# Kernel tuning notes

Measured on AMD Instinct MI355X. Metric: run time of the kernel, lower is better.

## Reference

```python
import jax, jax.numpy as jnp
import numpy as np

N, E, F, H, L = 10000, 200000, 28, 256, 6
NUM_ATOM, NUM_BOND = 100, 24

def ssp(x):
    # shifted softplus used by SchNet
    return jax.nn.softplus(x) - jnp.log(2.0)

def setup_inputs() -> dict:
    key = jax.random.key(0)
    ks = iter(jax.random.split(key, 64))
    def nrm(shape, scale=0.05):
        return jax.random.normal(next(ks), shape, dtype=jnp.float32) * scale
    inp = {}
    inp['atom_type'] = jax.random.randint(next(ks), (N,), 0, NUM_ATOM)
    inp['r_feat'] = jax.random.normal(next(ks), (N, F), dtype=jnp.float32)
    inp['p_feat'] = jax.random.normal(next(ks), (N, F), dtype=jnp.float32)
    inp['pos'] = jax.random.normal(next(ks), (N, 3), dtype=jnp.float32) * 3.0
    inp['edge_index'] = jax.random.randint(next(ks), (2, E), 0, N)
    inp['edge_type_r'] = jax.random.randint(next(ks), (E,), 0, NUM_BOND)
    inp['edge_type_p'] = jax.random.randint(next(ks), (E,), 0, NUM_BOND)
    # learned parameters
    inp['atom_emb_table'] = nrm((NUM_ATOM, H // 2), 1.0)
    inp['feat_W'] = nrm((F, H // 2))                       # atom_feat_embedding (no bias)
    inp['bond_emb_table'] = nrm((NUM_BOND, H), 1.0)        # edge encoder bond embedding
    inp['edge_mlp_W1'] = nrm((1, H)); inp['edge_mlp_b1'] = jnp.zeros((H,), jnp.float32)
    inp['edge_mlp_W2'] = nrm((H, H)); inp['edge_mlp_b2'] = jnp.zeros((H,), jnp.float32)
    inp['cat_W1'] = nrm((2 * H, H)); inp['cat_b1'] = jnp.zeros((H,), jnp.float32)
    inp['cat_W2'] = nrm((H, H)); inp['cat_b2'] = jnp.zeros((H,), jnp.float32)
    # SchNet interaction blocks, stacked over L layers
    inp['filt_W1'] = nrm((L, H, H)); inp['filt_b1'] = jnp.zeros((L, H), jnp.float32)
    inp['filt_W2'] = nrm((L, H, H)); inp['filt_b2'] = jnp.zeros((L, H), jnp.float32)
    inp['lin1_W'] = nrm((L, H, H))
    inp['lin2_W'] = nrm((L, H, H)); inp['lin2_b'] = jnp.zeros((L, H), jnp.float32)
    inp['lin3_W'] = nrm((L, H, H)); inp['lin3_b'] = jnp.zeros((L, H), jnp.float32)
    # grad_global_dist_mlp: 2H -> H -> H/2 -> 1
    inp['grad_W1'] = nrm((2 * H, H)); inp['grad_b1'] = jnp.zeros((H,), jnp.float32)
    inp['grad_W2'] = nrm((H, H // 2)); inp['grad_b2'] = jnp.zeros((H // 2,), jnp.float32)
    inp['grad_W3'] = nrm((H // 2, 1)); inp['grad_b3'] = jnp.zeros((1,), jnp.float32)
    return inp

def _forward(r_feat, p_feat, pos, atom_emb_table, feat_W, bond_emb_table,
             edge_mlp_W1, edge_mlp_b1, edge_mlp_W2, edge_mlp_b2,
             cat_W1, cat_b1, cat_W2, cat_b2,
             filt_W1, filt_b1, filt_W2, filt_b2,
             lin1_W, lin2_W, lin2_b, lin3_W, lin3_b,
             grad_W1, grad_b1, grad_W2, grad_b2, grad_W3, grad_b3,
             atom_type, edge_index, edge_type_r, edge_type_p):
    src, dst = edge_index[0], edge_index[1]
    # node embedding: z = [atom_emb + feat(r), feat(p) - feat(r)]
    ar = r_feat @ feat_W
    ap = p_feat @ feat_W
    z = jnp.concatenate([atom_emb_table[atom_type] + ar, ap - ar], axis=-1)  # (N, H)
    # edge lengths (E, 1)
    d = pos[src] - pos[dst]
    edge_length = jnp.sqrt(jnp.sum(d * d, axis=-1, keepdims=True) + 1e-12)
    # condensed edge embedding 'bond_w_d': mlp(d) * bond_emb(type), r/p branches, then edge_cat MLP
    d_emb = ssp(edge_length @ edge_mlp_W1 + edge_mlp_b1) @ edge_mlp_W2 + edge_mlp_b2  # (E, H)
    attr_r = d_emb * bond_emb_table[edge_type_r]
    attr_p = d_emb * bond_emb_table[edge_type_p]
    edge_attr = jax.nn.relu(jnp.concatenate([attr_r, attr_p], -1) @ cat_W1 + cat_b1) @ cat_W2 + cat_b2  # (E, H)
    # SchNet encoder: L CFConv interaction blocks with residual
    nn_ = z.shape[0]
    def layer(h, p):
        fW1, fb1, fW2, fb2, l1, l2, l2b, l3, l3b = p
        Wf = ssp(edge_attr @ fW1 + fb1) @ fW2 + fb2            # (E, H) continuous filters
        msg = (h @ l1)[src] * Wf                               # gather + modulate
        agg = jax.ops.segment_sum(msg, dst, num_segments=nn_)  # scatter-add to nodes
        return h + (ssp(agg @ l2 + l2b) @ l3 + l3b), None
    node_attr, _ = jax.lax.scan(layer, z, (filt_W1, filt_b1, filt_W2, filt_b2, lin1_W, lin2_W, lin2_b, lin3_W, lin3_b))
    # assemble_atom_pair_feature: [h_row * h_col, edge_attr] -> (E, 2H)
    h_pair = jnp.concatenate([node_attr[src] * node_attr[dst], edge_attr], axis=-1)
    h = jax.nn.relu(h_pair @ grad_W1 + grad_b1)
    h = jax.nn.relu(h @ grad_W2 + grad_b2)
    edge_inv = h @ grad_W3 + grad_b3                           # (E, 1)
    return edge_inv, edge_length

def reference(atom_type, r_feat, p_feat, pos, edge_index, edge_type_r, edge_type_p,
              atom_emb_table, feat_W, bond_emb_table,
              edge_mlp_W1, edge_mlp_b1, edge_mlp_W2, edge_mlp_b2,
              cat_W1, cat_b1, cat_W2, cat_b2,
              filt_W1, filt_b1, filt_W2, filt_b2,
              lin1_W, lin2_W, lin2_b, lin3_W, lin3_b,
              grad_W1, grad_b1, grad_W2, grad_b2, grad_W3, grad_b3):
    return _forward(r_feat, p_feat, pos, atom_emb_table, feat_W, bond_emb_table,
                    edge_mlp_W1, edge_mlp_b1, edge_mlp_W2, edge_mlp_b2,
                    cat_W1, cat_b1, cat_W2, cat_b2,
                    filt_W1, filt_b1, filt_W2, filt_b2,
                    lin1_W, lin2_W, lin2_b, lin3_W, lin3_b,
                    grad_W1, grad_b1, grad_W2, grad_b2, grad_W3, grad_b3,
                    atom_type, edge_index, edge_type_r, edge_type_p)
```

## Files before the change

kernel.cpp:

```cpp
#include <hip/hip_runtime.h>
#include <hip/hip_bf16.h>
#include <math.h>

#define HDIM 256

typedef unsigned short u16;
typedef short short8 __attribute__((ext_vector_type(8)));
typedef _Float16 f16x8 __attribute__((ext_vector_type(8)));
typedef float f32x4 __attribute__((ext_vector_type(4)));

__device__ __forceinline__ float sspf(float x) {
  const float LOG2E = 1.4426950408889634f, LN2 = 0.6931471805599453f;
  float t = exp2f(-fabsf(x) * LOG2E);
  return fmaxf(x, 0.f) + (log2f(1.f + t) - 1.f) * LN2;
}
__device__ __forceinline__ float bf2f(u16 u) {
  union { unsigned int i; float f; } x; x.i = ((unsigned int)u) << 16; return x.f;
}
__device__ __forceinline__ u16 f2bf(float f) {
  union { float f; unsigned int i; } x; x.f = f;
  unsigned int r = x.i + 0x7FFFu + ((x.i >> 16) & 1u);
  return (u16)(r >> 16);
}
__device__ __forceinline__ u16 f2h_bits(float f) {
  _Float16 h = (_Float16)f;
  return __builtin_bit_cast(unsigned short, h);
}
__device__ __forceinline__ float4 ld4f(const float* p) { return *(const float4*)p; }

__device__ __forceinline__ int iw_idx(int row, int col) {
  return row * 256 + ((((col >> 3) ^ (row & 7)) << 3) | (col & 7));
}
__device__ __forceinline__ int ir_idx(int row, int cchunk) {
  return row * 256 + ((cchunk ^ (row & 7)) << 3);
}

template<int DT>
__device__ __forceinline__ f32x4 mma(short8 a, short8 b, f32x4 c) {
  if constexpr (DT == 0)
    return __builtin_amdgcn_mfma_f32_16x16x32_bf16(a, b, c, 0, 0, 0);
  else
    return __builtin_amdgcn_mfma_f32_16x16x32_f16(__builtin_bit_cast(f16x8, a),
                                                  __builtin_bit_cast(f16x8, b), c, 0, 0, 0);
}

__device__ __forceinline__ void zacc(f32x4 (&acc)[4][4]) {
#pragma unroll
  for (int i = 0; i < 4; ++i)
#pragma unroll
    for (int j = 0; j < 4; ++j) { acc[i][j][0]=0.f; acc[i][j][1]=0.f; acc[i][j][2]=0.f; acc[i][j][3]=0.f; }
}

template<int NSTEPS, int BT_N, int NTW, int DT, bool WRAP8, typename ATR>
__device__ __forceinline__ void gemm44(f32x4 (&acc)[4][4], const u16* __restrict__ bt,
                                       const u16* __restrict__ inter,
                                       int w, int m, int quad, ATR atr) {
  short8 bf[2][NTW];
#pragma unroll
  for (int nt = 0; nt < NTW; ++nt)
    bf[0][nt] = *(const short8*)(bt + (w * (NTW * 16) + nt * 16 + m) * 32 + quad * 8);
#pragma unroll
  for (int ks = 0; ks < NSTEPS; ++ks) {
    const int cur = ks & 1, nxt = cur ^ 1;
    if (ks + 1 < NSTEPS) {
#pragma unroll
      for (int nt = 0; nt < NTW; ++nt)
        bf[nxt][nt] = *(const short8*)(bt + (size_t)(ks + 1) * (BT_N * 32)
                                       + (w * (NTW * 16) + nt * 16 + m) * 32 + quad * 8);
    }
    int kchunk = (WRAP8 ? (ks & 7) : ks) * 4 + quad;
#pragma unroll
    for (int mt = 0; mt < 4; ++mt) {
      short8 af = *(const short8*)&inter[ir_idx(mt * 16 + m, kchunk)];
      af = atr(mt, ks, af);
#pragma unroll
      for (int nt = 0; nt < NTW; ++nt)
        acc[mt][nt] = mma<DT>(af, bf[cur][nt], acc[mt][nt]);
    }
  }
}

template<int NTW, int ACT, int OF>
__device__ __forceinline__ void store_inter44(u16* inter, int w, int m, int quad,
                                              const f32x4 (&acc)[4][4], const float* bias) {
#pragma unroll
  for (int mt = 0; mt < 4; ++mt)
#pragma unroll
    for (int nt = 0; nt < NTW; ++nt) {
      int col = w * (NTW * 16) + nt * 16 + m;
      float bv = bias[col];
#pragma unroll
      for (int r = 0; r < 4; ++r) {
        int row = mt * 16 + quad * 4 + r;
        float x = acc[mt][nt][r] + bv;
        if (ACT == 1) x = fmaxf(x, 0.f);
        else if (ACT == 2) x = sspf(x);
        inter[iw_idx(row, col)] = (OF == 0) ? f2bf(x) : f2h_bits(x);
      }
    }
}

__device__ __forceinline__ void copy_out(u16* C, int row0, const u16* inter, int t) {
#pragma unroll
  for (int c = 0; c < 8; ++c) {
    int idx = c * 256 + t;
    int row = idx >> 5, c8 = idx & 31;
    int src = (c8 ^ (row & 7)) << 3;
    *(short8*)(C + (size_t)(row0 + row) * HDIM + c8 * 8) = *(const short8*)&inter[row * 256 + src];
  }
}

template<int NTW, int ACT, int CM>
__device__ __forceinline__ void store_node44(float* C, int row0, int w, int m, int quad,
                                             const f32x4 (&acc)[4][4], const float* bias, int M) {
#pragma unroll
  for (int mt = 0; mt < 4; ++mt)
#pragma unroll
    for (int nt = 0; nt < NTW; ++nt) {
      int col = w * (NTW * 16) + nt * 16 + m;
      float bv = bias ? bias[col] : 0.f;
#pragma unroll
      for (int r = 0; r < 4; ++r) {
        int row = row0 + mt * 16 + quad * 4 + r;
        if (row < M) {
          float x = acc[mt][nt][r] + bv;
          if (ACT == 2) x = sspf(x);
          size_t idx = (size_t)row * HDIM + col;
          if (CM == 1) x += C[idx];
          C[idx] = x;
        }
      }
    }
}

struct EncArgs {
  const int* se_e; const float* lenp; const float* W1; const float* b1;
  const u16* btA; const float* bA;
  const float* bondT; const int* etr; const int* etp;
  const u16* btB; const float* bB;
  const u16* btC; const float* bC;
  u16* outp;
};
__global__ __launch_bounds__(256, 3) void encoder_k(EncArgs a) {
  __shared__ u16 inter[64 * 256];
  __shared__ u16 bondL[24 * 264];
  const int t = threadIdx.x;
  const int w = t >> 6, lane = t & 63, m = lane & 15, quad = lane >> 4;
  const int row0 = blockIdx.x * 64;
  auto idt = [](int, int, short8 v) { return v; };

  for (int i = t; i < 24 * 256; i += 256) {
    int r = i >> 8, c = i & 255;
    bondL[r * 264 + c] = f2h_bits(a.bondT[r * 256 + c]);
  }
  int brv[4], bpv[4];
#pragma unroll
  for (int mt = 0; mt < 4; ++mt) {
    int eo = a.se_e[row0 + mt * 16 + m];
    brv[mt] = a.etr[eo]; bpv[mt] = a.etp[eo];
  }
  {
    int row = t >> 2;
    float len = a.lenp[a.se_e[row0 + row]];
#pragma unroll
    for (int c = 0; c < 8; ++c) {
      int chunk = (t & 3) + c * 4, k = chunk * 8;
      float4 w0 = ld4f(a.W1 + k), w1 = ld4f(a.W1 + k + 4);
      float4 c0 = ld4f(a.b1 + k), c1 = ld4f(a.b1 + k + 4);
      short8 v;
      v[0] = (short)f2bf(sspf(len * w0.x + c0.x)); v[1] = (short)f2bf(sspf(len * w0.y + c0.y));
      v[2] = (short)f2bf(sspf(len * w0.z + c0.z)); v[3] = (short)f2bf(sspf(len * w0.w + c0.w));
      v[4] = (short)f2bf(sspf(len * w1.x + c1.x)); v[5] = (short)f2bf(sspf(len * w1.y + c1.y));
      v[6] = (short)f2bf(sspf(len * w1.z + c1.z)); v[7] = (short)f2bf(sspf(len * w1.w + c1.w));
      *(short8*)&inter[row * 256 + ((chunk ^ (row & 7)) << 3)] = v;
    }
  }
  __syncthreads();
  f32x4 acc[4][4];
  zacc(acc);
  gemm44<8, 256, 4, 0, false>(acc, a.btA, inter, w, m, quad, idt);
  __syncthreads();
  store_inter44<4, 0, 1>(inter, w, m, quad, acc, a.bA);
  __syncthreads();
  zacc(acc);
  auto atrB = [&](int mt, int ks, short8 v) -> short8 {
    int k2 = (ks & 7) * 32 + quad * 8;
    int et = (ks < 8) ? brv[mt] : bpv[mt];
    f16x8 dv = __builtin_bit_cast(f16x8, v);
    f16x8 bd = __builtin_bit_cast(f16x8, *(const short8*)&bondL[et * 264 + k2]);
    return __builtin_bit_cast(short8, dv * bd);
  };
  gemm44<16, 256, 4, 1, true>(acc, a.btB, inter, w, m, quad, atrB);
  __syncthreads();
  store_inter44<4, 1, 0>(inter, w, m, quad, acc, a.bB);
  __syncthreads();
  zacc(acc);
  gemm44<8, 256, 4, 0, false>(acc, a.btC, inter, w, m, quad, idt);
  __syncthreads();
  store_inter44<4, 0, 0>(inter, w, m, quad, acc, a.bC);
  __syncthreads();
  copy_out(a.outp, row0, inter, t);
}

struct FL1Args {
  const u16* eA; const u16* bt1; const float* b1; const u16* bt2; const float* b2; u16* Wf;
  int EBlocks;
  const float* h; const u16* btL; float* hh; int M;
};
__global__ __launch_bounds__(256, 3) void fl1_k(FL1Args a) {
  __shared__ u16 inter[64 * 256];
  const int t = threadIdx.x;
  const int w = t >> 6, lane = t & 63, m = lane & 15, quad = lane >> 4;
  auto idt = [](int, int, short8 v) { return v; };
  if ((int)blockIdx.x < a.EBlocks) {
    const int row0 = blockIdx.x * 64;
    {
      int row = t >> 2;
#pragma unroll
      for (int c = 0; c < 8; ++c) {
        int chunk = (t & 3) + c * 4;
        short8 v = *(const short8*)(a.eA + (size_t)(row0 + row) * HDIM + chunk * 8);
        *(short8*)&inter[row * 256 + ((chunk ^ (row & 7)) << 3)] = v;
      }
    }
    __syncthreads();
    f32x4 acc[4][4];
    zacc(acc);
    gemm44<8, 256, 4, 0, false>(acc, a.bt1, inter, w, m, quad, idt);
    __syncthreads();
    store_inter44<4, 2, 0>(inter, w, m, quad, acc, a.b1);
    __syncthreads();
    zacc(acc);
    gemm44<8, 256, 4, 0, false>(acc, a.bt2, inter, w, m, quad, idt);
    __syncthreads();
    store_inter44<4, 0, 0>(inter, w, m, quad, acc, a.b2);
    __syncthreads();
    copy_out(a.Wf, row0, inter, t);
  } else {
    const int row0 = ((int)blockIdx.x - a.EBlocks) * 64;
    {
      int row = t >> 2, grow = row0 + row;
#pragma unroll
      for (int c = 0; c < 8; ++c) {
        int chunk = (t & 3) + c * 4, k = chunk * 8;
        short8 v;
        if (grow < a.M) {
          const float* p = a.h + (size_t)grow * HDIM + k;
          float4 x0 = ld4f(p), x1 = ld4f(p + 4);
          v[0]=(short)f2bf(x0.x); v[1]=(short)f2bf(x0.y); v[2]=(short)f2bf(x0.z); v[3]=(short)f2bf(x0.w);
          v[4]=(short)f2bf(x1.x); v[5]=(short)f2bf(x1.y); v[6]=(short)f2bf(x1.z); v[7]=(short)f2bf(x1.w);
        } else { v = short8{0,0,0,0,0,0,0,0}; }
        *(short8*)&inter[row * 256 + ((chunk ^ (row & 7)) << 3)] = v;
      }
    }
    __syncthreads();
    f32x4 acc[4][4];
    zacc(acc);
    gemm44<8, 256, 4, 0, false>(acc, a.btL, inter, w, m, quad, idt);
    store_node44<4, 0, 0>(a.hh, row0, w, m, quad, acc, nullptr, a.M);
  }
}

struct GradArgs {
  const float* h; const int* se_src; const int* se_dst; const int* se_e;
  const u16* eA; const u16* bt1; const float* b1; const u16* bt2; const float* b2;
  const float* W3; const float* b3; float* outp;
};
__global__ __launch_bounds__(256, 3) void gradf_k(GradArgs a) {
  __shared__ u16 inter[64 * 256];
  const int t = threadIdx.x;
  const int w = t >> 6, lane = t & 63, m = lane & 15, quad = lane >> 4;
  const int row0 = blockIdx.x * 64;
  auto idt = [](int, int, short8 v) { return v; };
  {
    int row = t >> 2;
    int s = a.se_src[row0 + row], d = a.se_dst[row0 + row];
#pragma unroll
    for (int c = 0; c < 8; ++c) {
      int chunk = (t & 3) + c * 4, k = chunk * 8;
      const float* xp = a.h + (size_t)s * HDIM + k;
      const float* yp = a.h + (size_t)d * HDIM + k;
      float4 x0 = ld4f(xp), x1 = ld4f(xp + 4);
      float4 y0 = ld4f(yp), y1 = ld4f(yp + 4);
      short8 v;
      v[0] = (short)f2bf(x0.x * y0.x); v[1] = (short)f2bf(x0.y * y0.y);
      v[2] = (short)f2bf(x0.z * y0.z); v[3] = (short)f2bf(x0.w * y0.w);
      v[4] = (short)f2bf(x1.x * y1.x); v[5] = (short)f2bf(x1.y * y1.y);
      v[6] = (short)f2bf(x1.z * y1.z); v[7] = (short)f2bf(x1.w * y1.w);
      *(short8*)&inter[row * 256 + ((chunk ^ (row & 7)) << 3)] = v;
    }
  }
  __syncthreads();
  f32x4 acc[4][4];
  zacc(acc);
  gemm44<8, 256, 4, 0, false>(acc, a.bt1, inter, w, m, quad, idt);
  __syncthreads();
  {
    int row = t >> 2;
#pragma unroll
    for (int c = 0; c < 8; ++c) {
      int chunk = (t & 3) + c * 4;
      short8 v = *(const short8*)(a.eA + (size_t)(row0 + row) * HDIM + chunk * 8);
      *(short8*)&inter[row * 256 + ((chunk ^ (row & 7)) << 3)] = v;
    }
  }
  __syncthreads();
  gemm44<8, 256, 4, 0, false>(acc, a.bt1 + 8 * 256 * 32, inter, w, m, quad, idt);
  __syncthreads();
  store_inter44<4, 1, 0>(inter, w, m, quad, acc, a.b1);
  __syncthreads();
  zacc(acc);
  gemm44<8, 128, 2, 0, false>(acc, a.bt2, inter, w, m, quad, idt);
  float p[4][4];
#pragma unroll
  for (int mt = 0; mt < 4; ++mt) { p[mt][0]=0.f; p[mt][1]=0.f; p[mt][2]=0.f; p[mt][3]=0.f; }
#pragma unroll
  for (int mt = 0; mt < 4; ++mt)
#pragma unroll
    for (int nt = 0; nt < 2; ++nt) {
      int col = w * 32 + nt * 16 + m;
      float w3 = a.W3[col], bv = a.b2[col];
#pragma unroll
      for (int r = 0; r < 4; ++r) p[mt][r] += fmaxf(acc[mt][nt][r] + bv, 0.f) * w3;
    }
  __syncthreads();
  float* red = (float*)inter;
#pragma unroll
  for (int mt = 0; mt < 4; ++mt)
#pragma unroll
    for (int r = 0; r < 4; ++r)
      red[(mt * 16 + quad * 4 + r) * 68 + w * 16 + m] = p[mt][r];
  __syncthreads();
  if (t < 64) {
    float s = a.b3[0];
#pragma unroll
    for (int i = 0; i < 64; ++i) s += red[t * 68 + i];
    a.outp[a.se_e[row0 + t]] = s;
  }
}

struct Lin23Args { const float* A; const u16* bt2; const float* b2; const u16* bt3; const float* b3; float* C; int M; };
__global__ __launch_bounds__(256, 3) void lin23_k(Lin23Args a) {
  __shared__ u16 inter[64 * 256];
  const int t = threadIdx.x;
  const int w = t >> 6, lane = t & 63, m = lane & 15, quad = lane >> 4;
  const int row0 = blockIdx.x * 64;
  auto idt = [](int, int, short8 v) { return v; };
  {
    int row = t >> 2, grow = row0 + row;
#pragma unroll
    for (int c = 0; c < 8; ++c) {
      int chunk = (t & 3) + c * 4, k = chunk * 8;
      short8 v;
      if (grow < a.M) {
        const float* p = a.A + (size_t)grow * HDIM + k;
        float4 x0 = ld4f(p), x1 = ld4f(p + 4);
        v[0]=(short)f2bf(x0.x); v[1]=(short)f2bf(x0.y); v[2]=(short)f2bf(x0.z); v[3]=(short)f2bf(x0.w);
        v[4]=(short)f2bf(x1.x); v[5]=(short)f2bf(x1.y); v[6]=(short)f2bf(x1.z); v[7]=(short)f2bf(x1.w);
      } else { v = short8{0,0,0,0,0,0,0,0}; }
      *(short8*)&inter[row * 256 + ((chunk ^ (row & 7)) << 3)] = v;
    }
  }
  __syncthreads();
  f32x4 acc[4][4];
  zacc(acc);
  gemm44<8, 256, 4, 0, false>(acc, a.bt2, inter, w, m, quad, idt);
  __syncthreads();
  store_inter44<4, 2, 0>(inter, w, m, quad, acc, a.b2);
  __syncthreads();
  zacc(acc);
  gemm44<8, 256, 4, 0, false>(acc, a.bt3, inter, w, m, quad, idt);
  store_node44<4, 0, 1>(a.C, row0, w, m, quad, acc, a.b3, a.M);
}

struct WTDesc { const float* src; u16* dst; int K; int Nshift; int fmt; };
struct WTList { WTDesc d[35]; };
__global__ __launch_bounds__(256) void wtrans_k(WTList wl) {
  WTDesc e = wl.d[blockIdx.y];
  int total = e.K << e.Nshift;
  int idx = blockIdx.x * 256 + threadIdx.x;
  if (idx >= total) return;
  int k = idx >> e.Nshift;
  int n = idx & ((1 << e.Nshift) - 1);
  float v = e.src[idx];
  e.dst[((size_t)(k >> 5) << (e.Nshift + 5)) + n * 32 + (k & 31)] = e.fmt ? f2h_bits(v) : f2bf(v);
}

__global__ void node_embed_k(const int* atom_type, const float* r_feat, const float* p_feat,
                             const float* emb, const float* fW, float* z, int N, int F) {
  int n = blockIdx.x;
  int j = threadIdx.x;
  __shared__ float rr[32], pp[32];
  if (j < F) { rr[j] = r_feat[(size_t)n * F + j]; pp[j] = p_feat[(size_t)n * F + j]; }
  __syncthreads();
  float ar = 0.f, ap = 0.f;
  for (int f = 0; f < F; ++f) {
    float wv = fW[f * 128 + j];
    ar += rr[f] * wv;
    ap += pp[f] * wv;
  }
  int at = atom_type[n];
  z[(size_t)n * HDIM + j] = emb[at * 128 + j] + ar;
  z[(size_t)n * HDIM + 128 + j] = ap - ar;
}

__global__ void edge_geom_k(const float* pos, const int* src, const int* dst, float* len_out, int E) {
  int e = blockIdx.x * blockDim.x + threadIdx.x;
  if (e >= E) return;
  int s = src[e], d = dst[e];
  float dx = pos[s * 3 + 0] - pos[d * 3 + 0];
  float dy = pos[s * 3 + 1] - pos[d * 3 + 1];
  float dz = pos[s * 3 + 2] - pos[d * 3 + 2];
  len_out[e] = sqrtf(dx * dx + dy * dy + dz * dz + 1e-12f);
}

__global__ void zero_k(float4* p, int n4) {
  int i = blockIdx.x * 256 + threadIdx.x;
  if (i < n4) p[i] = make_float4(0.f, 0.f, 0.f, 0.f);
}
__global__ void zero_int_k(int* p, int n) {
  int i = blockIdx.x * 256 + threadIdx.x;
  if (i < n) p[i] = 0;
}
__global__ void hist_k(const int* dst, int* cnt, int E) {
  int e = blockIdx.x * 256 + threadIdx.x;
  if (e < E) atomicAdd(&cnt[dst[e]], 1);
}
__global__ __launch_bounds__(256) void scan_k(const int* cnt, int* rowstart, int N) {
  __shared__ int part[256];
  int t = threadIdx.x;
  int chunk = (N + 255) / 256;
  int lo = t * chunk, hi = lo + chunk; if (hi > N) hi = N; if (lo > N) lo = N;
  int s = 0;
  for (int i = lo; i < hi; ++i) s += cnt[i];
  part[t] = s;
  __syncthreads();
  for (int off = 1; off < 256; off <<= 1) {
    int v = (t >= off) ? part[t - off] : 0;
    __syncthreads();
    part[t] += v;
    __syncthreads();
  }
  int run = (t == 0) ? 0 : part[t - 1];
  for (int i = lo; i < hi; ++i) { rowstart[i] = run; run += cnt[i]; }
  if (t == 255) rowstart[N] = run;
}
__global__ void fill_k(const int* src, const int* dst, const int* rowstart, int* cursor,
                       int* se_src, int* se_dst, int* se_e, int E) {
  int e = blockIdx.x * 256 + threadIdx.x;
  if (e >= E) return;
  int d = dst[e];
  int p = atomicAdd(&cursor[d], 1);
  int idx = rowstart[d] + p;
  se_src[idx] = src[e];
  se_dst[idx] = d;
  se_e[idx] = e;
}

__global__ __launch_bounds__(256) void gather_k(const float* hh, const u16* Wf,
                                                const int* se_src, const int* rowstart,
                                                float* agg, int N) {
  int n = blockIdx.x;
  int j = threadIdx.x;
  int s0 = rowstart[n], s1 = rowstart[n + 1];
  float acc = 0.f;
  for (int i = s0; i < s1; ++i)
    acc += hh[(size_t)se_src[i] * HDIM + j] * bf2f(Wf[(size_t)i * HDIM + j]);
  agg[(size_t)n * HDIM + j] = acc;
}

extern "C" void kernel_launch(void* const* d_in, const int* in_sizes, int n_in,
                              void* d_out, int out_size, void* d_ws, size_t ws_size,
                              hipStream_t stream) {
  const int* atom_type = (const int*)d_in[0];
  const float* r_feat  = (const float*)d_in[1];
  const float* p_feat  = (const float*)d_in[2];
  const float* pos     = (const float*)d_in[3];
  const int* eidx      = (const int*)d_in[4];
  const int* etype_r   = (const int*)d_in[5];
  const int* etype_p   = (const int*)d_in[6];
  const float* atom_emb = (const float*)d_in[7];
  const float* feat_W   = (const float*)d_in[8];
  const float* bondT    = (const float*)d_in[9];
  const float* e_W1     = (const float*)d_in[10];
  const float* e_b1     = (const float*)d_in[11];
  const float* e_W2     = (const float*)d_in[12];
  const float* e_b2     = (const float*)d_in[13];
  const float* cat_W1   = (const float*)d_in[14];
  const float* cat_b1   = (const float*)d_in[15];
  const float* cat_W2   = (const float*)d_in[16];
  const float* cat_b2   = (const float*)d_in[17];
  const float* filt_W1  = (const float*)d_in[18];
  const float* filt_b1  = (const float*)d_in[19];
  const float* filt_W2  = (const float*)d_in[20];
  const float* filt_b2  = (const float*)d_in[21];
  const float* lin1_W   = (const float*)d_in[22];
  const float* lin2_W   = (const float*)d_in[23];
  const float* lin2_b   = (const float*)d_in[24];
  const float* lin3_W   = (const float*)d_in[25];
  const float* lin3_b   = (const float*)d_in[26];
  const float* grad_W1  = (const float*)d_in[27];
  const float* grad_b1  = (const float*)d_in[28];
  const float* grad_W2  = (const float*)d_in[29];
  const float* grad_b2  = (const float*)d_in[30];
  const float* grad_W3  = (const float*)d_in[31];
  const float* grad_b3  = (const float*)d_in[32];

  const int N = in_sizes[0];
  const int F = in_sizes[1] / N;
  const int E = in_sizes[4] / 2;
  const int L = in_sizes[18] / (HDIM * HDIM);
  const int* srcI = eidx;
  const int* dstI = eidx + E;
  float* out = (float*)d_out;

  const size_t BT_ELEMS = (size_t)(32 * 65536 + 2 * 131072 + 32768);
  size_t need = 2 * (size_t)E * HDIM * 2 + 3 * (size_t)N * HDIM * 4 + BT_ELEMS * 2
              + (size_t)(3 * E + 3 * N + 1) * 4 + 64;
  if (ws_size < need) {
    int n4 = (out_size + 3) / 4;
    zero_k<<<(n4 + 255) / 256, 256, 0, stream>>>((float4*)d_out, n4);
    return;
  }
  char* base = (char*)d_ws;
  u16* eA = (u16*)base; base += (size_t)E * HDIM * 2;
  u16* Wf = (u16*)base; base += (size_t)E * HDIM * 2;
  float* h   = (float*)base; base += (size_t)N * HDIM * 4;
  float* hh  = (float*)base; base += (size_t)N * HDIM * 4;
  float* agg = (float*)base; base += (size_t)N * HDIM * 4;
  u16* bt = (u16*)base; base += BT_ELEMS * 2;
  int* se_src = (int*)base; base += (size_t)E * 4;
  int* se_dst = (int*)base; base += (size_t)E * 4;
  int* se_e   = (int*)base; base += (size_t)E * 4;
  int* cnt    = (int*)base; base += (size_t)N * 4;
  int* cursor = (int*)base; base += (size_t)N * 4;
  int* rowstart = (int*)base; base += ((size_t)N + 1) * 4;

  size_t off = 0;
  u16* bt_eW2  = bt + off; off += 65536;
  u16* bt_cat1 = bt + off; off += 131072;
  u16* bt_cat2 = bt + off; off += 65536;
  u16* bt_f1[6]; u16* bt_f2[6]; u16* bt_l1[6]; u16* bt_l2[6]; u16* bt_l3[6];
  for (int l = 0; l < 6; ++l) { bt_f1[l] = bt + off; off += 65536; }
  for (int l = 0; l < 6; ++l) { bt_f2[l] = bt + off; off += 65536; }
  for (int l = 0; l < 6; ++l) { bt_l1[l] = bt + off; off += 65536; }
  for (int l = 0; l < 6; ++l) { bt_l2[l] = bt + off; off += 65536; }
  for (int l = 0; l < 6; ++l) { bt_l3[l] = bt + off; off += 65536; }
  u16* bt_g1 = bt + off; off += 131072;
  u16* bt_g2 = bt + off; off += 32768;

  WTList wl;
  int wi = 0;
  wl.d[wi++] = WTDesc{e_W2, bt_eW2, 256, 8, 0};
  wl.d[wi++] = WTDesc{cat_W1, bt_cat1, 512, 8, 1};
  wl.d[wi++] = WTDesc{cat_W2, bt_cat2, 256, 8, 0};
  for (int l = 0; l < 6; ++l) wl.d[wi++] = WTDesc{filt_W1 + (size_t)l * 65536, bt_f1[l], 256, 8, 0};
  for (int l = 0; l < 6; ++l) wl.d[wi++] = WTDesc{filt_W2 + (size_t)l * 65536, bt_f2[l], 256, 8, 0};
  for (int l = 0; l < 6; ++l) wl.d[wi++] = WTDesc{lin1_W + (size_t)l * 65536, bt_l1[l], 256, 8, 0};
  for (int l = 0; l < 6; ++l) wl.d[wi++] = WTDesc{lin2_W + (size_t)l * 65536, bt_l2[l], 256, 8, 0};
  for (int l = 0; l < 6; ++l) wl.d[wi++] = WTDesc{lin3_W + (size_t)l * 65536, bt_l3[l], 256, 8, 0};
  wl.d[wi++] = WTDesc{grad_W1, bt_g1, 512, 8, 0};
  wl.d[wi++] = WTDesc{grad_W2, bt_g2, 256, 7, 0};
  wtrans_k<<<dim3(512, 35), 256, 0, stream>>>(wl);

  const int EB = E / 64;
  const int NBK = (N + 63) / 64;
  const int EBLK = (E + 255) / 256;

  zero_int_k<<<(2 * N + 255) / 256, 256, 0, stream>>>(cnt, 2 * N);
  hist_k<<<EBLK, 256, 0, stream>>>(dstI, cnt, E);
  scan_k<<<1, 256, 0, stream>>>(cnt, rowstart, N);
  fill_k<<<EBLK, 256, 0, stream>>>(srcI, dstI, rowstart, cursor, se_src, se_dst, se_e, E);

  node_embed_k<<<N, 128, 0, stream>>>(atom_type, r_feat, p_feat, atom_emb, feat_W, h, N, F);
  edge_geom_k<<<EBLK, 256, 0, stream>>>(pos, srcI, dstI, out + E, E);

  EncArgs ea;
  ea.se_e = se_e; ea.lenp = out + E; ea.W1 = e_W1; ea.b1 = e_b1;
  ea.btA = bt_eW2; ea.bA = e_b2;
  ea.bondT = bondT; ea.etr = etype_r; ea.etp = etype_p;
  ea.btB = bt_cat1; ea.bB = cat_b1;
  ea.btC = bt_cat2; ea.bC = cat_b2;
  ea.outp = eA;
  encoder_k<<<EB, 256, 0, stream>>>(ea);

  for (int l = 0; l < L; ++l) {
    const size_t bo = (size_t)l * HDIM;
    FL1Args fl;
    fl.eA = eA; fl.bt1 = bt_f1[l]; fl.b1 = filt_b1 + bo; fl.bt2 = bt_f2[l]; fl.b2 = filt_b2 + bo;
    fl.Wf = Wf; fl.EBlocks = EB;
    fl.h = h; fl.btL = bt_l1[l]; fl.hh = hh; fl.M = N;
    fl1_k<<<EB + NBK, 256, 0, stream>>>(fl);
    gather_k<<<N, 256, 0, stream>>>(hh, Wf, se_src, rowstart, agg, N);
    Lin23Args l23{agg, bt_l2[l], lin2_b + bo, bt_l3[l], lin3_b + bo, h, N};
    lin23_k<<<NBK, 256, 0, stream>>>(l23);
  }

  GradArgs ga;
  ga.h = h; ga.se_src = se_src; ga.se_dst = se_dst; ga.se_e = se_e;
  ga.eA = eA; ga.bt1 = bt_g1; ga.b1 = grad_b1; ga.bt2 = bt_g2; ga.b2 = grad_b2;
  ga.W3 = grad_W3; ga.b3 = grad_b3; ga.outp = out;
  gradf_k<<<EB, 256, 0, stream>>>(ga);
}
```

Before: 1.614 ms.

## Fuse neighbor gather into lin2/lin3 kernel and drop shared bond table

Replaces the separate per-node gather kernel and lin23 kernel with one kernel that aggregates messages for 64 nodes into shared memory, then runs both GEMMs. This removes the fp32 agg buffer round trip and one launch per layer. The encoder now reads bond embeddings straight from global memory with per-use fp16 conversion instead of staging them in LDS, and the occupancy hints in launch bounds are removed. The fused gather runs on far fewer blocks with serial per-row loops, which risks poor parallelism and latency hiding.

```diff
diff --git a/kernel.cpp b/kernel.cpp
--- a/kernel.cpp
+++ b/kernel.cpp
@@ -27,6 +27,10 @@
   return __builtin_bit_cast(unsigned short, h);
 }
 __device__ __forceinline__ float4 ld4f(const float* p) { return *(const float4*)p; }
+__device__ __forceinline__ float4 ld4b(const u16* p) {
+  ushort4 u = *(const ushort4*)p;
+  return make_float4(bf2f(u.x), bf2f(u.y), bf2f(u.z), bf2f(u.w));
+}
 
 __device__ __forceinline__ int iw_idx(int row, int col) {
   return row * 256 + ((((col >> 3) ^ (row & 7)) << 3) | (col & 7));
@@ -141,18 +145,13 @@
   const u16* btC; const float* bC;
   u16* outp;
 };
-__global__ __launch_bounds__(256, 3) void encoder_k(EncArgs a) {
+__global__ __launch_bounds__(256) void encoder_k(EncArgs a) {
   __shared__ u16 inter[64 * 256];
-  __shared__ u16 bondL[24 * 264];
   const int t = threadIdx.x;
   const int w = t >> 6, lane = t & 63, m = lane & 15, quad = lane >> 4;
   const int row0 = blockIdx.x * 64;
   auto idt = [](int, int, short8 v) { return v; };
 
-  for (int i = t; i < 24 * 256; i += 256) {
-    int r = i >> 8, c = i & 255;
-    bondL[r * 264 + c] = f2h_bits(a.bondT[r * 256 + c]);
-  }
   int brv[4], bpv[4];
 #pragma unroll
   for (int mt = 0; mt < 4; ++mt) {
@@ -186,8 +185,12 @@
   auto atrB = [&](int mt, int ks, short8 v) -> short8 {
     int k2 = (ks & 7) * 32 + quad * 8;
     int et = (ks < 8) ? brv[mt] : bpv[mt];
+    const float* brow = a.bondT + (size_t)et * 256 + k2;
+    float4 q0 = ld4f(brow), q1 = ld4f(brow + 4);
+    f16x8 bd;
+    bd[0] = (_Float16)q0.x; bd[1] = (_Float16)q0.y; bd[2] = (_Float16)q0.z; bd[3] = (_Float16)q0.w;
+    bd[4] = (_Float16)q1.x; bd[5] = (_Float16)q1.y; bd[6] = (_Float16)q1.z; bd[7] = (_Float16)q1.w;
     f16x8 dv = __builtin_bit_cast(f16x8, v);
-    f16x8 bd = __builtin_bit_cast(f16x8, *(const short8*)&bondL[et * 264 + k2]);
     return __builtin_bit_cast(short8, dv * bd);
   };
   gemm44<16, 256, 4, 1, true>(acc, a.btB, inter, w, m, quad, atrB);
@@ -207,7 +210,7 @@
   int EBlocks;
   const float* h; const u16* btL; float* hh; int M;
 };
-__global__ __launch_bounds__(256, 3) void fl1_k(FL1Args a) {
+__global__ __launch_bounds__(256) void fl1_k(FL1Args a) {
   __shared__ u16 inter[64 * 256];
   const int t = threadIdx.x;
   const int w = t >> 6, lane = t & 63, m = lane & 15, quad = lane >> 4;
@@ -261,12 +264,60 @@
   }
 }
 
+struct GL23Args {
+  const float* hh; const u16* Wf; const int* se_src; const int* rowstart;
+  const u16* bt2; const float* b2; const u16* bt3; const float* b3; float* C; int M;
+};
+__global__ __launch_bounds__(256) void glin23_k(GL23Args a) {
+  __shared__ u16 inter[64 * 256];
+  __shared__ int rsl[65];
+  const int t = threadIdx.x;
+  const int w = t >> 6, lane = t & 63, m = lane & 15, quad = lane >> 4;
+  const int row0 = blockIdx.x * 64;
+  auto idt = [](int, int, short8 v) { return v; };
+  if (t < 65) {
+    int nn = row0 + t;
+    rsl[t] = a.rowstart[nn > a.M ? a.M : nn];
+  }
+  __syncthreads();
+  {
+    int cbase = lane * 4;
+    int wr = ((((cbase) >> 3) ^ 0) << 3) | (cbase & 7);
+    (void)wr;
+#pragma unroll 1
+    for (int rr = 0; rr < 16; ++rr) {
+      int r = w * 16 + rr;
+      int s0 = rsl[r], s1 = rsl[r + 1];
+      float a0 = 0.f, a1 = 0.f, a2 = 0.f, a3 = 0.f;
+      for (int i = s0; i < s1; ++i) {
+        int src = a.se_src[i];
+        float4 hv = ld4f(a.hh + (size_t)src * HDIM + cbase);
+        float4 wv = ld4b(a.Wf + (size_t)i * HDIM + cbase);
+        a0 += hv.x * wv.x; a1 += hv.y * wv.y; a2 += hv.z * wv.z; a3 += hv.w * wv.w;
+      }
+      int base = r * 256 + ((((cbase >> 3) ^ (r & 7)) << 3) | (cbase & 7));
+      ushort4 o; o.x = f2bf(a0); o.y = f2bf(a1); o.z = f2bf(a2); o.w = f2bf(a3);
+      *(ushort4*)&inter[base] = o;
+    }
+  }
+  __syncthreads();
+  f32x4 acc[4][4];
+  zacc(acc);
+  gemm44<8, 256, 4, 0, false>(acc, a.bt2, inter, w, m, quad, idt);
+  __syncthreads();
+  store_inter44<4, 2, 0>(inter, w, m, quad, acc, a.b2);
+  __syncthreads();
+  zacc(acc);
+  gemm44<8, 256, 4, 0, false>(acc, a.bt3, inter, w, m, quad, idt);
+  store_node44<4, 0, 1>(a.C, row0, w, m, quad, acc, a.b3, a.M);
+}
+
 struct GradArgs {
   const float* h; const int* se_src; const int* se_dst; const int* se_e;
   const u16* eA; const u16* bt1; const float* b1; const u16* bt2; const float* b2;
   const float* W3; const float* b3; float* outp;
 };
-__global__ __launch_bounds__(256, 3) void gradf_k(GradArgs a) {
+__global__ __launch_bounds__(256) void gradf_k(GradArgs a) {
   __shared__ u16 inter[64 * 256];
   const int t = threadIdx.x;
   const int w = t >> 6, lane = t & 63, m = lane & 15, quad = lane >> 4;
@@ -339,40 +390,6 @@
   }
 }
 
-struct Lin23Args { const float* A; const u16* bt2; const float* b2; const u16* bt3; const float* b3; float* C; int M; };
-__global__ __launch_bounds__(256, 3) void lin23_k(Lin23Args a) {
-  __shared__ u16 inter[64 * 256];
-  const int t = threadIdx.x;
-  const int w = t >> 6, lane = t & 63, m = lane & 15, quad = lane >> 4;
-  const int row0 = blockIdx.x * 64;
-  auto idt = [](int, int, short8 v) { return v; };
-  {
-    int row = t >> 2, grow = row0 + row;
-#pragma unroll
-    for (int c = 0; c < 8; ++c) {
-      int chunk = (t & 3) + c * 4, k = chunk * 8;
-      short8 v;
-      if (grow < a.M) {
-        const float* p = a.A + (size_t)grow * HDIM + k;
-        float4 x0 = ld4f(p), x1 = ld4f(p + 4);
-        v[0]=(short)f2bf(x0.x); v[1]=(short)f2bf(x0.y); v[2]=(short)f2bf(x0.z); v[3]=(short)f2bf(x0.w);
-        v[4]=(short)f2bf(x1.x); v[5]=(short)f2bf(x1.y); v[6]=(short)f2bf(x1.z); v[7]=(short)f2bf(x1.w);
-      } else { v = short8{0,0,0,0,0,0,0,0}; }
-      *(short8*)&inter[row * 256 + ((chunk ^ (row & 7)) << 3)] = v;
-    }
-  }
-  __syncthreads();
-  f32x4 acc[4][4];
-  zacc(acc);
-  gemm44<8, 256, 4, 0, false>(acc, a.bt2, inter, w, m, quad, idt);
-  __syncthreads();
-  store_inter44<4, 2, 0>(inter, w, m, quad, acc, a.b2);
-  __syncthreads();
-  zacc(acc);
-  gemm44<8, 256, 4, 0, false>(acc, a.bt3, inter, w, m, quad, idt);
-  store_node44<4, 0, 1>(a.C, row0, w, m, quad, acc, a.b3, a.M);
-}
-
 struct WTDesc { const float* src; u16* dst; int K; int Nshift; int fmt; };
 struct WTList { WTDesc d[35]; };
 __global__ __launch_bounds__(256) void wtrans_k(WTList wl) {
@@ -455,18 +472,6 @@
   se_src[idx] = src[e];
   se_dst[idx] = d;
   se_e[idx] = e;
-}
-
-__global__ __launch_bounds__(256) void gather_k(const float* hh, const u16* Wf,
-                                                const int* se_src, const int* rowstart,
-                                                float* agg, int N) {
-  int n = blockIdx.x;
-  int j = threadIdx.x;
-  int s0 = rowstart[n], s1 = rowstart[n + 1];
-  float acc = 0.f;
-  for (int i = s0; i < s1; ++i)
-    acc += hh[(size_t)se_src[i] * HDIM + j] * bf2f(Wf[(size_t)i * HDIM + j]);
-  agg[(size_t)n * HDIM + j] = acc;
 }
 
 extern "C" void kernel_launch(void* const* d_in, const int* in_sizes, int n_in,
@@ -515,7 +520,7 @@
   float* out = (float*)d_out;
 
   const size_t BT_ELEMS = (size_t)(32 * 65536 + 2 * 131072 + 32768);
-  size_t need = 2 * (size_t)E * HDIM * 2 + 3 * (size_t)N * HDIM * 4 + BT_ELEMS * 2
+  size_t need = 2 * (size_t)E * HDIM * 2 + 2 * (size_t)N * HDIM * 4 + BT_ELEMS * 2
               + (size_t)(3 * E + 3 * N + 1) * 4 + 64;
   if (ws_size < need) {
     int n4 = (out_size + 3) / 4;
@@ -527,7 +532,6 @@
   u16* Wf = (u16*)base; base += (size_t)E * HDIM * 2;
   float* h   = (float*)base; base += (size_t)N * HDIM * 4;
   float* hh  = (float*)base; base += (size_t)N * HDIM * 4;
-  float* agg = (float*)base; base += (size_t)N * HDIM * 4;
   u16* bt = (u16*)base; base += BT_ELEMS * 2;
   int* se_src = (int*)base; base += (size_t)E * 4;
   int* se_dst = (int*)base; base += (size_t)E * 4;
@@ -591,9 +595,11 @@
     fl.Wf = Wf; fl.EBlocks = EB;
     fl.h = h; fl.btL = bt_l1[l]; fl.hh = hh; fl.M = N;
     fl1_k<<<EB + NBK, 256, 0, stream>>>(fl);
-    gather_k<<<N, 256, 0, stream>>>(hh, Wf, se_src, rowstart, agg, N);
-    Lin23Args l23{agg, bt_l2[l], lin2_b + bo, bt_l3[l], lin3_b + bo, h, N};
-    lin23_k<<<NBK, 256, 0, stream>>>(l23);
+    GL23Args gl;
+    gl.hh = hh; gl.Wf = Wf; gl.se_src = se_src; gl.rowstart = rowstart;
+    gl.bt2 = bt_l2[l]; gl.b2 = lin2_b + bo; gl.bt3 = bt_l3[l]; gl.b3 = lin3_b + bo;
+    gl.C = h; gl.M = N;
+    glin23_k<<<NBK, 256, 0, stream>>>(gl);
   }
 
   GradArgs ga;
```

Measured after the change: 2.672 ms. +65.5%, slower.
